# Optimization experiments

Measured on AMD Instinct MI355X. Metric: run time of the kernel, lower is better.

The kernel has to match this reference:

```python
import jax, jax.numpy as jnp
import numpy as np

D_MODEL = 1024
N_HEADS = 16
D_FF = 4096
D_K = D_MODEL // N_HEADS


def _ln(x, g, b, eps=1e-5):
    mu = jnp.mean(x, axis=-1, keepdims=True)
    var = jnp.mean(jnp.square(x - mu), axis=-1, keepdims=True)
    return (x - mu) * jax.lax.rsqrt(var + eps) * g + b


def setup_inputs() -> dict:
    key = jax.random.key(0)
    ks = jax.random.split(key, 16)
    s = 0.02
    inp = {
        "x": jax.random.normal(ks[0], (2, 2048, D_MODEL), dtype=jnp.float32),
        "Wq": jax.random.normal(ks[1], (D_MODEL, D_MODEL), dtype=jnp.float32) * s,
        "bq": jnp.zeros((D_MODEL,), jnp.float32),
        "Wk": jax.random.normal(ks[2], (D_MODEL, D_MODEL), dtype=jnp.float32) * s,
        "bk": jnp.zeros((D_MODEL,), jnp.float32),
        "Wv": jax.random.normal(ks[3], (D_MODEL, D_MODEL), dtype=jnp.float32) * s,
        "bv": jnp.zeros((D_MODEL,), jnp.float32),
        "Wo": jax.random.normal(ks[4], (D_MODEL, D_MODEL), dtype=jnp.float32) * s,
        "bo": jnp.zeros((D_MODEL,), jnp.float32),
        "W1": jax.random.normal(ks[5], (D_MODEL, D_FF), dtype=jnp.float32) * s,
        "b1": jnp.zeros((D_FF,), jnp.float32),
        "W2": jax.random.normal(ks[6], (D_FF, D_MODEL), dtype=jnp.float32) * s,
        "b2": jnp.zeros((D_MODEL,), jnp.float32),
        "g1": jnp.ones((D_MODEL,), jnp.float32),
        "be1": jnp.zeros((D_MODEL,), jnp.float32),
        "g2": jnp.ones((D_MODEL,), jnp.float32),
        "be2": jnp.zeros((D_MODEL,), jnp.float32),
    }
    return inp


def reference(x, Wq, bq, Wk, bk, Wv, bv, Wo, bo, W1, b1, W2, b2, g1, be1, g2, be2):
    B, L, D = x.shape
    # QKV projections -> [B, H, L, d_k]
    q = (x @ Wq + bq).reshape(B, L, N_HEADS, D_K).transpose(0, 2, 1, 3)
    k = (x @ Wk + bk).reshape(B, L, N_HEADS, D_K).transpose(0, 2, 1, 3)
    v = (x @ Wv + bv).reshape(B, L, N_HEADS, D_K).transpose(0, 2, 1, 3)
    scores = jnp.einsum("bhqd,bhkd->bhqk", q, k) / jnp.sqrt(jnp.float32(D_K))
    attn = jax.nn.softmax(scores, axis=-1)
    ctx = jnp.einsum("bhqk,bhkd->bhqd", attn, v)
    ctx = ctx.transpose(0, 2, 1, 3).reshape(B, L, D)
    attn_out = ctx @ Wo + bo
    # residual + LN1
    h = _ln(x + attn_out, g1, be1)
    # FFN (exact GELU, matching torch F.gelu default)
    ff = jax.nn.gelu(h @ W1 + b1, approximate=False) @ W2 + b2
    return _ln(h + ff, g2, be2)
```

## Files before the change

### kernel.cpp

```cpp
#include <hip/hip_runtime.h>
#include <cmath>


typedef unsigned short u16;
typedef unsigned int u32;
typedef __attribute__((ext_vector_type(8))) __bf16 bf16x8;
typedef __attribute__((ext_vector_type(4))) float f32x4;

#define MFMA16(a, b, c) __builtin_amdgcn_mfma_f32_16x16x32_bf16(a, b, c, 0, 0, 0)

__device__ __forceinline__ u16 f2bf(float f) {
  u32 u = __builtin_bit_cast(u32, f);
  u += 0x7fffu + ((u >> 16) & 1u);
  return (u16)(u >> 16);
}

__device__ __forceinline__ u32 packtrunc(float lo, float hi) {
#if __has_builtin(__builtin_amdgcn_perm)
  return __builtin_amdgcn_perm(__builtin_bit_cast(u32, hi),
                               __builtin_bit_cast(u32, lo), 0x07060302u);
#else
  return (__builtin_bit_cast(u32, lo) >> 16) |
         (__builtin_bit_cast(u32, hi) & 0xFFFF0000u);
#endif
}

__device__ __forceinline__ bf16x8 ld_frag(const u16* p) {
  return __builtin_bit_cast(bf16x8, *(const uint4*)p);
}

__device__ __forceinline__ float fexp2(float x) {
#if __has_builtin(__builtin_amdgcn_exp2f)
  return __builtin_amdgcn_exp2f(x);
#else
  return exp2f(x);
#endif
}

__device__ __forceinline__ float frcp(float x) {
#if __has_builtin(__builtin_amdgcn_rcpf)
  return __builtin_amdgcn_rcpf(x);
#else
  return 1.0f / x;
#endif
}

__device__ __forceinline__ float gelu_f(float v) {
  float x = v * 0.70710678118654752f;
  float a = fabsf(x);
  float t = frcp(fmaf(0.3275911f, a, 1.0f));
  float p = fmaf(1.061405429f, t, -1.453152027f);
  p = fmaf(p, t, 1.421413741f);
  p = fmaf(p, t, -0.284496736f);
  p = fmaf(p, t, 0.254829592f);
  p = p * t;
  float e = fexp2(-a * a * 1.4426950408889634f);
  float er = copysignf(1.0f - p * e, x);
  return 0.5f * v * (1.0f + er);
}

__device__ __forceinline__ void gload16(const u16* g, u16* l) {
  __builtin_amdgcn_global_load_lds(
      (const __attribute__((address_space(1))) void*)g,
      (__attribute__((address_space(3))) void*)l, 16, 0, 0);
}

#define WAITVL(N) asm volatile("s_waitcnt vmcnt(" #N ") lgkmcnt(0)" ::: "memory")
#define BAR() do { __builtin_amdgcn_s_barrier(); asm volatile("" ::: "memory"); } while (0)

__global__ __launch_bounds__(256) void prep_k(
    const float* __restrict__ x,
    const float* __restrict__ Wq, const float* __restrict__ Wk,
    const float* __restrict__ Wv, const float* __restrict__ Wo,
    const float* __restrict__ W1, const float* __restrict__ W2,
    u16* __restrict__ xb, u16* __restrict__ wqkvT, u16* __restrict__ woT,
    u16* __restrict__ w1T, u16* __restrict__ w2T) {
  const int z = blockIdx.z;
  if (z >= 12) {
    long i = (((long)(z - 12) * 1024 + blockIdx.y * 32 + blockIdx.x) * 256 +
              threadIdx.x) * 4;
    float4 v = *(const float4*)(x + i);
    ushort4 o;
    o.x = f2bf(v.x); o.y = f2bf(v.y); o.z = f2bf(v.z); o.w = f2bf(v.w);
    *(ushort4*)(xb + i) = o;
    return;
  }
  __shared__ float tile[32][33];
  const float* src;
  u16* dst;
  int R, C, r0, c0;
  if (z < 4) {
    src = (z == 0) ? Wq : (z == 1) ? Wk : (z == 2) ? Wv : Wo;
    dst = (z < 3) ? (wqkvT + (size_t)z * 1024 * 1024) : woT;
    R = 1024; C = 1024;
    r0 = blockIdx.y * 32; c0 = blockIdx.x * 32;
  } else if (z < 8) {
    src = W1; dst = w1T; R = 1024; C = 4096;
    r0 = blockIdx.y * 32; c0 = (z - 4) * 1024 + blockIdx.x * 32;
  } else {
    src = W2; dst = w2T; R = 4096; C = 1024;
    r0 = (z - 8) * 1024 + blockIdx.y * 32; c0 = blockIdx.x * 32;
  }
  int tx = threadIdx.x & 31, ty = threadIdx.x >> 5;
#pragma unroll
  for (int i = 0; i < 4; i++)
    tile[ty + 8 * i][tx] = src[(long)(r0 + ty + 8 * i) * C + c0 + tx];
  __syncthreads();
#pragma unroll
  for (int i = 0; i < 4; i++)
    dst[(long)(c0 + ty + 8 * i) * R + r0 + tx] = f2bf(tile[tx][ty + 8 * i]);
}

template <int MODE>
__global__ __launch_bounds__(512, 2) void gemm256_8p(
    const u16* __restrict__ A, const u16* __restrict__ BT,
    int N, int lda, int ldb, int K,
    const float* __restrict__ bias, u16* __restrict__ outB,
    u16* __restrict__ qd, u16* __restrict__ kd, u16* __restrict__ vTd,
    const float* __restrict__ bq, const float* __restrict__ bk,
    const float* __restrict__ bv) {
  __shared__ u16 As[2][2][128 * 64];
  __shared__ u16 Bs[2][2][128 * 64];
  const int tid = threadIdx.x;
  const int wave = tid >> 6, lane = tid & 63, quad = lane >> 4, l16 = lane & 15;
  const int wm = wave >> 2, wn = wave & 3;
  const int gx = gridDim.x;
  int flat = blockIdx.y * gx + blockIdx.x;
  const int cpx = (gx * gridDim.y) >> 3;
  flat = (flat & 7) * cpx + (flat >> 3);
  const int m0 = (flat / gx) * 256, n0 = (flat % gx) * 256;
  const int KT = K >> 6;

  const int srow8 = lane >> 3;
  const int sseg8 = (lane & 7) ^ srow8;
  const u16* aSrc = A + (long)(m0 + wave * 8 + srow8) * lda + sseg8 * 8;
  const u16* bSrc = BT + (long)(n0 + wave * 8 + srow8) * ldb + sseg8 * 8;

  auto stageA = [&](int tt, int h) {
    const u16* s = aSrc + (long)(h * 128) * lda + tt * 64;
    u16* d = &As[tt & 1][h][wave * 512];
    gload16(s, d);
    gload16(s + 64 * (long)lda, d + 4096);
  };
  auto stageB = [&](int tt, int h) {
    const u16* s = bSrc + (long)(h * 128) * ldb + tt * 64;
    u16* d = &Bs[tt & 1][h][wave * 512];
    gload16(s, d);
    gload16(s + 64 * (long)ldb, d + 4096);
  };

  const int s7 = l16 & 7;
  int lrB[4];
#pragma unroll
  for (int nf = 0; nf < 4; nf++) lrB[nf] = (wn & 1) * 64 + nf * 16 + l16;

  f32x4 acc[8][4] = {};

  stageA(0, 0); stageA(0, 1);
  stageB(0, 0); stageB(0, 1);
  stageA(1, 0); stageA(1, 1);
  stageB(1, 0); stageB(1, 1);
  WAITVL(8);
  BAR();

#pragma unroll 1
  for (int t = 0; t < KT; ++t) {
    const int buf = t & 1;
    const u16* Ah = &As[buf][wm][0];
    const u16* Bh = &Bs[buf][wn >> 1][0];
    bf16x8 bfr[4][2];
#pragma unroll
    for (int q = 0; q < 4; ++q) {
      if (q == 0) {
#pragma unroll
        for (int nf = 0; nf < 4; nf++)
#pragma unroll
          for (int kk = 0; kk < 2; kk++)
            bfr[nf][kk] =
                ld_frag(Bh + lrB[nf] * 64 + (((kk * 4 + quad) ^ s7) * 8));
      }
      bf16x8 af[2][2];
#pragma unroll
      for (int mfl = 0; mfl < 2; mfl++)
#pragma unroll
        for (int kk = 0; kk < 2; kk++)
          af[mfl][kk] = ld_frag(Ah + (q * 32 + mfl * 16 + l16) * 64 +
                                (((kk * 4 + quad) ^ s7) * 8));
      if (q == 0) { if (t >= 1 && t + 1 < KT) stageA(t + 1, 0); }
      else if (q == 1) { if (t >= 1 && t + 1 < KT) stageA(t + 1, 1); }
      else if (q == 2) { if (t + 2 < KT) stageB(t + 2, 0); }
      else {
        if (t + 2 < KT) stageB(t + 2, 1);
        if (t < KT - 2) { WAITVL(4); } else { WAITVL(0); }
      }
      BAR();
      __builtin_amdgcn_s_setprio(1);
#pragma unroll
      for (int kk = 0; kk < 2; kk++)
#pragma unroll
        for (int mfl = 0; mfl < 2; mfl++)
#pragma unroll
          for (int nf = 0; nf < 4; nf++)
            acc[q * 2 + mfl][nf] =
                MFMA16(af[mfl][kk], bfr[nf][kk], acc[q * 2 + mfl][nf]);
      __builtin_amdgcn_s_setprio(0);
      BAR();
    }
  }

  if (MODE == 0) {
    const int nbase = n0 + wn * 64;
    const int mat = nbase >> 10;
    const float* bp = (mat == 0) ? bq : ((mat == 1) ? bk : bv);
    float bb[4];
    int hh0[4], dd0[4];
#pragma unroll
    for (int nf = 0; nf < 4; nf++) {
      int nn = (nbase + nf * 16 + l16) & 1023;
      bb[nf] = bp[nn];
      hh0[nf] = nn >> 6;
      dd0[nf] = nn & 63;
    }
    if (mat < 2) {
#pragma unroll
      for (int mf = 0; mf < 8; mf++) {
#pragma unroll
        for (int r = 0; r < 4; r++) {
          int mr = m0 + wm * 128 + mf * 16 + quad * 4 + r;
          int bI = mr >> 11, ll = mr & 2047;
#pragma unroll
          for (int nf = 0; nf < 4; nf++) {
            float v = acc[mf][nf][r] + bb[nf];
            long idx = ((long)((bI * 16 + hh0[nf]) * 2048 + ll)) * 64 + dd0[nf];
            if (mat == 0) {
              qd[idx] = f2bf(v * 0.18033688011112043f);
            } else {
              kd[idx] = f2bf(v);
            }
          }
        }
      }
    } else {
#pragma unroll
      for (int nf = 0; nf < 4; nf++) {
#pragma unroll
        for (int mf = 0; mf < 8; mf++) {
#pragma unroll
          for (int r = 0; r < 4; r++) {
            int mr = m0 + wm * 128 + mf * 16 + quad * 4 + r;
            int bI = mr >> 11, ll = mr & 2047;
            float v = acc[mf][nf][r] + bb[nf];
            vTd[((long)((bI * 16 + hh0[nf]) * 64 + dd0[nf])) * 2048 + ll] = f2bf(v);
          }
        }
      }
    }
  } else {
    float bb[4];
#pragma unroll
    for (int nf = 0; nf < 4; nf++) bb[nf] = bias[n0 + wn * 64 + nf * 16 + l16];
#pragma unroll
    for (int mf = 0; mf < 8; mf++) {
#pragma unroll
      for (int r = 0; r < 4; r++) {
        int mr = m0 + wm * 128 + mf * 16 + quad * 4 + r;
        u16* orow = outB + (long)mr * N + n0 + wn * 64 + l16;
#pragma unroll
        for (int nf = 0; nf < 4; nf++)
          orow[nf * 16] = f2bf(gelu_f(acc[mf][nf][r] + bb[nf]));
      }
    }
  }
}

template <int MODE>
__global__ __launch_bounds__(256, 3) void gemm128_k(
    const u16* __restrict__ A, const u16* __restrict__ BT,
    int N, int lda, int ldb, int Kc,
    const float* __restrict__ bias, float* __restrict__ outF,
    u16* __restrict__ outB, float* __restrict__ p1) {
  __shared__ u16 As[3][128 * 32];
  __shared__ u16 Bs[3][128 * 32];
  const int tid = threadIdx.x;
  const int wave = tid >> 6, lane = tid & 63, quad = lane >> 4, l16 = lane & 15;
  const int wm = wave >> 1, wn = wave & 1;
  const int gx = gridDim.x;
  int flat = blockIdx.y * gx + blockIdx.x;
  const int cpx = (gx * gridDim.y) >> 3;
  flat = (flat & 7) * cpx + (flat >> 3);
  const int m0 = (flat / gx) * 128, n0 = (flat % gx) * 128;
  const int kz = blockIdx.z;
  const long kofs = (long)kz * Kc;
  const int KT = Kc >> 5;

  const int srow = lane >> 2;
  const int sseg = (lane & 3) ^ (srow & 3);
  const u16* aS = A + (long)(m0 + wave * 32 + srow) * lda + kofs + sseg * 8;
  const u16* bS = BT + (long)(n0 + wave * 32 + srow) * ldb + kofs + sseg * 8;

  auto stage = [&](int sb, int s) {
    const u16* pa = aS + (long)s * 32;
    gload16(pa, &As[sb][wave * 1024]);
    gload16(pa + 16 * (long)lda, &As[sb][wave * 1024 + 512]);
    const u16* pb = bS + (long)s * 32;
    gload16(pb, &Bs[sb][wave * 1024]);
    gload16(pb + 16 * (long)ldb, &Bs[sb][wave * 1024 + 512]);
  };

  int aro[4], bro[4];
#pragma unroll
  for (int f = 0; f < 4; f++) {
    int ra = wm * 64 + f * 16 + l16;
    aro[f] = ra * 32 + ((quad ^ (ra & 3)) * 8);
    int rb = wn * 64 + f * 16 + l16;
    bro[f] = rb * 32 + ((quad ^ (rb & 3)) * 8);
  }

  f32x4 acc[4][4] = {};

  stage(0, 0);
  stage(1, 1);
  int buf = 0;
#pragma unroll 1
  for (int t = 0; t < KT; ++t) {
    if (t < KT - 1) { WAITVL(4); } else { WAITVL(0); }
    BAR();
    bf16x8 af[4], bfr[4];
#pragma unroll
    for (int i = 0; i < 4; i++) af[i] = ld_frag(&As[buf][aro[i]]);
#pragma unroll
    for (int i = 0; i < 4; i++) bfr[i] = ld_frag(&Bs[buf][bro[i]]);
    if (t + 2 < KT) {
      int nb = buf + 2; if (nb >= 3) nb -= 3;
      stage(nb, t + 2);
    }
    __builtin_amdgcn_s_setprio(1);
#pragma unroll
    for (int mf = 0; mf < 4; mf++)
#pragma unroll
      for (int nf = 0; nf < 4; nf++)
        acc[mf][nf] = MFMA16(af[mf], bfr[nf], acc[mf][nf]);
    __builtin_amdgcn_s_setprio(0);
    if (++buf == 3) buf = 0;
  }

  {
    float* sl = (kz == 0) ? outF : p1;
#pragma unroll
    for (int mf = 0; mf < 4; mf++) {
#pragma unroll
      for (int r = 0; r < 4; r++) {
        int mr = m0 + wm * 64 + mf * 16 + quad * 4 + r;
        float* orow = sl + (long)mr * N + n0 + wn * 64 + l16;
#pragma unroll
        for (int nf = 0; nf < 4; nf++) orow[nf * 16] = acc[mf][nf][r];
      }
    }
  }
}

__global__ __launch_bounds__(256, 3) void attn_k(const u16* __restrict__ qd,
                                                 const u16* __restrict__ kd,
                                                 const u16* __restrict__ vTd,
                                                 u16* __restrict__ ctx) {
  __shared__ u16 Ks[2][64 * 64];
  __shared__ u16 Vs[2][64 * 64];
  __shared__ __align__(16) u16 P[4][32][72];
  const int tid = threadIdx.x;
  const int wave = tid >> 6, lane = tid & 63, quad = lane >> 4, l16 = lane & 15;
  const int bh = blockIdx.y;
  const u16* Q = qd + (long)bh * 2048 * 64;
  const u16* Kp = kd + (long)bh * 2048 * 64;
  const u16* Vt = vTd + (long)bh * 64 * 2048;
  const int qbase = blockIdx.x * 128 + wave * 32;

  bf16x8 qf[2][2];
#pragma unroll
  for (int qs = 0; qs < 2; qs++) {
    qf[qs][0] = ld_frag(Q + (qbase + qs * 16 + l16) * 64 + quad * 8);
    qf[qs][1] = ld_frag(Q + (qbase + qs * 16 + l16) * 64 + 32 + quad * 8);
  }

  f32x4 o[2][4] = {};
  float m[2] = {-1e30f, -1e30f}, l[2] = {0.f, 0.f};

  const int srow = lane >> 3;
  const int sx = (lane & 7) ^ srow;
  const int kr0 = wave * 16 + srow;
  const int kr1 = wave * 16 + 8 + srow;

  const int fs0 = ((0 * 4 + quad) ^ (l16 & 7)) * 8;
  const int fs1 = ((1 * 4 + quad) ^ (l16 & 7)) * 8;

  auto stage = [&](int buf, int j0) {
    gload16(Kp + (long)(j0 + kr0) * 64 + sx * 8, &Ks[buf][(wave * 2 + 0) * 512]);
    gload16(Kp + (long)(j0 + kr1) * 64 + sx * 8, &Ks[buf][(wave * 2 + 1) * 512]);
    gload16(Vt + (long)kr0 * 2048 + j0 + sx * 8, &Vs[buf][(wave * 2 + 0) * 512]);
    gload16(Vt + (long)kr1 * 2048 + j0 + sx * 8, &Vs[buf][(wave * 2 + 1) * 512]);
  };

  stage(0, 0);

#pragma unroll 1
  for (int j0 = 0; j0 < 2048; j0 += 64) {
    const int buf = (j0 >> 6) & 1;
    __syncthreads();
    if (j0 + 64 < 2048) stage(buf ^ 1, j0 + 64);

    const u16* kb = &Ks[buf][0];
    f32x4 st[2][4];
#pragma unroll
    for (int f = 0; f < 4; f++) {
      bf16x8 k0 = ld_frag(kb + (f * 16 + l16) * 64 + fs0);
      bf16x8 k1 = ld_frag(kb + (f * 16 + l16) * 64 + fs1);
      f32x4 s0 = {}, s1 = {};
      s0 = MFMA16(k0, qf[0][0], s0); s0 = MFMA16(k1, qf[0][1], s0);
      s1 = MFMA16(k0, qf[1][0], s1); s1 = MFMA16(k1, qf[1][1], s1);
      st[0][f] = s0; st[1][f] = s1;
    }

#pragma unroll
    for (int qs = 0; qs < 2; qs++) {
      float mx = -1e30f;
#pragma unroll
      for (int f = 0; f < 4; f++)
        mx = fmaxf(mx, fmaxf(fmaxf(st[qs][f][0], st[qs][f][1]),
                             fmaxf(st[qs][f][2], st[qs][f][3])));
      mx = fmaxf(mx, __shfl_xor(mx, 16));
      mx = fmaxf(mx, __shfl_xor(mx, 32));
      if (__any(mx > m[qs] + 8.0f)) {
        float mn = fmaxf(m[qs], mx);
        float al = fexp2(m[qs] - mn);
        m[qs] = mn;
        l[qs] *= al;
#pragma unroll
        for (int nt = 0; nt < 4; nt++) {
          o[qs][nt][0] *= al; o[qs][nt][1] *= al;
          o[qs][nt][2] *= al; o[qs][nt][3] *= al;
        }
      }
      float sm = 0.f;
      u16* prow = &P[wave][qs * 16 + l16][0];
#pragma unroll
      for (int f = 0; f < 4; f++) {
        float p0 = fexp2(st[qs][f][0] - m[qs]);
        float p1 = fexp2(st[qs][f][1] - m[qs]);
        float p2 = fexp2(st[qs][f][2] - m[qs]);
        float p3 = fexp2(st[qs][f][3] - m[qs]);
        sm += (p0 + p1) + (p2 + p3);
        uint2 u;
        u.x = packtrunc(p0, p1);
        u.y = packtrunc(p2, p3);
        *(uint2*)(prow + f * 16 + quad * 4) = u;
      }
      sm += __shfl_xor(sm, 16);
      sm += __shfl_xor(sm, 32);
      l[qs] += sm;
    }
    __asm__ volatile("s_waitcnt lgkmcnt(0)" ::: "memory");

    const u16* vb = &Vs[buf][0];
    bf16x8 vf[4][2];
#pragma unroll
    for (int nt = 0; nt < 4; nt++) {
      vf[nt][0] = ld_frag(vb + (nt * 16 + l16) * 64 + fs0);
      vf[nt][1] = ld_frag(vb + (nt * 16 + l16) * 64 + fs1);
    }
#pragma unroll
    for (int qs = 0; qs < 2; qs++) {
      const u16* prow = &P[wave][qs * 16 + l16][0];
#pragma unroll
      for (int kh = 0; kh < 2; kh++) {
        bf16x8 pf = ld_frag(prow + kh * 32 + quad * 8);
#pragma unroll
        for (int nt = 0; nt < 4; nt++)
          o[qs][nt] = MFMA16(vf[nt][kh], pf, o[qs][nt]);
      }
    }
  }

  const int bI = bh >> 4, hh = bh & 15;
#pragma unroll
  for (int qs = 0; qs < 2; qs++) {
    const float rl = 1.0f / l[qs];
    const long row = (long)(bI * 2048 + qbase + qs * 16 + l16);
#pragma unroll
    for (int nt = 0; nt < 4; nt++) {
      ushort4 w;
      w.x = f2bf(o[qs][nt][0] * rl);
      w.y = f2bf(o[qs][nt][1] * rl);
      w.z = f2bf(o[qs][nt][2] * rl);
      w.w = f2bf(o[qs][nt][3] * rl);
      *(ushort4*)(ctx + row * 1024 + hh * 64 + nt * 16 + quad * 4) = w;
    }
  }
}

__global__ __launch_bounds__(256) void ln2sb_k(const float* __restrict__ a,
                                               const float* __restrict__ q0,
                                               const float* __restrict__ q1,
                                               const float* __restrict__ bias,
                                               const float* __restrict__ g,
                                               const float* __restrict__ be,
                                               float* __restrict__ outF,
                                               u16* __restrict__ outB) {
  const int row = blockIdx.x, tid = threadIdx.x;
  const long base = (long)row * 1024;
  float v[4], s = 0.f, sq = 0.f;
#pragma unroll
  for (int i = 0; i < 4; i++) {
    int c = i * 256 + tid;
    float ff = q0[base + c] + q1[base + c] + bias[c];
    v[i] = a[base + c] + ff;
    s += v[i];
    sq += v[i] * v[i];
  }
#pragma unroll
  for (int off = 1; off < 64; off <<= 1) {
    s += __shfl_xor(s, off);
    sq += __shfl_xor(sq, off);
  }
  __shared__ float red[10];
  int wave = tid >> 6, lane = tid & 63;
  if (lane == 0) { red[wave * 2] = s; red[wave * 2 + 1] = sq; }
  __syncthreads();
  if (tid == 0) {
    float S = red[0] + red[2] + red[4] + red[6];
    float Q = red[1] + red[3] + red[5] + red[7];
    float mu = S * (1.0f / 1024.0f);
    float var = Q * (1.0f / 1024.0f) - mu * mu;
    red[8] = mu;
    red[9] = rsqrtf(var + 1e-5f);
  }
  __syncthreads();
  float mu = red[8], rstd = red[9];
#pragma unroll
  for (int i = 0; i < 4; i++) {
    int c = i * 256 + tid;
    float o = (v[i] - mu) * rstd * g[c] + be[c];
    outF[base + c] = o;
    if (outB) outB[base + c] = f2bf(o);
  }
}

extern "C" void kernel_launch(void* const* d_in, const int* in_sizes, int n_in,
                              void* d_out, int out_size, void* d_ws, size_t ws_size,
                              hipStream_t stream) {
  const float* x  = (const float*)d_in[0];
  const float* Wq = (const float*)d_in[1];  const float* bq = (const float*)d_in[2];
  const float* Wk = (const float*)d_in[3];  const float* bk = (const float*)d_in[4];
  const float* Wv = (const float*)d_in[5];  const float* bv = (const float*)d_in[6];
  const float* Wo = (const float*)d_in[7];  const float* bo = (const float*)d_in[8];
  const float* W1 = (const float*)d_in[9];  const float* b1 = (const float*)d_in[10];
  const float* W2 = (const float*)d_in[11]; const float* b2 = (const float*)d_in[12];
  const float* g1 = (const float*)d_in[13]; const float* be1 = (const float*)d_in[14];
  const float* g2 = (const float*)d_in[15]; const float* be2 = (const float*)d_in[16];

  char* ws = (char*)d_ws;
  size_t off = 0;
  auto alloc = [&](size_t bytes) {
    size_t o = off;
    off += (bytes + 255) & ~(size_t)255;
    return o;
  };
  u16*   xb     = (u16*)(ws + alloc(4096UL * 1024 * 2));
  u16*   wqkvT  = (u16*)(ws + alloc(3072UL * 1024 * 2));
  u16*   woT    = (u16*)(ws + alloc(1024UL * 1024 * 2));
  u16*   w1T    = (u16*)(ws + alloc(4096UL * 1024 * 2));
  u16*   w2T    = (u16*)(ws + alloc(1024UL * 4096 * 2));
  u16*   qb     = (u16*)(ws + alloc(32UL * 2048 * 64 * 2));
  u16*   kb     = (u16*)(ws + alloc(32UL * 2048 * 64 * 2));
  u16*   vTb    = (u16*)(ws + alloc(32UL * 64 * 2048 * 2));
  u16*   ctx    = (u16*)(ws + alloc(4096UL * 1024 * 2));
  float* attnO  = (float*)(ws + alloc(4096UL * 1024 * 4));
  float* h      = (float*)(ws + alloc(4096UL * 1024 * 4));
  u16*   hb     = (u16*)(ws + alloc(4096UL * 1024 * 2));
  u16*   ff1    = (u16*)(ws + alloc(4096UL * 4096 * 2));
  float* ff2    = (float*)(ws + alloc(4096UL * 1024 * 4));
  if (off > ws_size) return;

  float* wl0 = attnO;
  float* wl1 = ff2;
  float* sl0 = ff2;
  float* sl1 = attnO;

  prep_k<<<dim3(32, 32, 16), 256, 0, stream>>>(x, Wq, Wk, Wv, Wo, W1, W2,
                                               xb, wqkvT, woT, w1T, w2T);
  gemm256_8p<0><<<dim3(12, 16), 512, 0, stream>>>(
      xb, wqkvT, 3072, 1024, 1024, 1024,
      nullptr, nullptr, qb, kb, vTb, bq, bk, bv);
  attn_k<<<dim3(16, 32), 256, 0, stream>>>(qb, kb, vTb, ctx);
  gemm128_k<3><<<dim3(8, 32, 2), 256, 0, stream>>>(
      ctx, woT, 1024, 1024, 1024, 512,
      nullptr, wl0, nullptr, wl1);
  ln2sb_k<<<4096, 256, 0, stream>>>(x, wl0, wl1, bo, g1, be1, h, hb);
  gemm256_8p<2><<<dim3(16, 16), 512, 0, stream>>>(
      hb, w1T, 4096, 1024, 1024, 1024,
      b1, ff1, nullptr, nullptr, nullptr, nullptr, nullptr, nullptr);
  gemm128_k<3><<<dim3(8, 32, 2), 256, 0, stream>>>(
      ff1, w2T, 1024, 4096, 4096, 2048,
      nullptr, sl0, nullptr, sl1);
  ln2sb_k<<<4096, 256, 0, stream>>>(h, sl0, sl1, b2, g2, be2,
                                    (float*)d_out, nullptr);
}
```

Measured before the change: 356.5 us.

## Split-K W2 GEMM with 256-tile kernel and retile attention to 16-row waves

The FFN down-projection moves from the 128-tile split-K-by-2 kernel to the 256x256 eight-wave GEMM with a 4-way K split. Its fp32 partials are written into four buffers, reusing the dead q and vT buffers, and a new LayerNorm kernel sums all four. The attention kernel now runs 512 threads with 16 query rows per wave instead of 32, so each block has 8 waves for latency hiding. The trade-off is that K/V fragments are reused across fewer rows, and the split-K GEMM writes and reads more partial-sum traffic.

```diff
diff --git a/kernel.cpp b/kernel.cpp
--- a/kernel.cpp
+++ b/kernel.cpp
@@ -114,8 +114,10 @@
 template <int MODE>
 __global__ __launch_bounds__(512, 2) void gemm256_8p(
     const u16* __restrict__ A, const u16* __restrict__ BT,
-    int N, int lda, int ldb, int K,
+    int N, int lda, int ldb, int Kc,
     const float* __restrict__ bias, u16* __restrict__ outB,
+    float* __restrict__ outF, float* __restrict__ p1,
+    float* __restrict__ p2, float* __restrict__ p3,
     u16* __restrict__ qd, u16* __restrict__ kd, u16* __restrict__ vTd,
     const float* __restrict__ bq, const float* __restrict__ bk,
     const float* __restrict__ bv) {
@@ -129,12 +131,14 @@
   const int cpx = (gx * gridDim.y) >> 3;
   flat = (flat & 7) * cpx + (flat >> 3);
   const int m0 = (flat / gx) * 256, n0 = (flat % gx) * 256;
-  const int KT = K >> 6;
+  const int kz = blockIdx.z;
+  const long kofs = (long)kz * Kc;
+  const int KT = Kc >> 6;
 
   const int srow8 = lane >> 3;
   const int sseg8 = (lane & 7) ^ srow8;
-  const u16* aSrc = A + (long)(m0 + wave * 8 + srow8) * lda + sseg8 * 8;
-  const u16* bSrc = BT + (long)(n0 + wave * 8 + srow8) * ldb + sseg8 * 8;
+  const u16* aSrc = A + (long)(m0 + wave * 8 + srow8) * lda + kofs + sseg8 * 8;
+  const u16* bSrc = BT + (long)(n0 + wave * 8 + srow8) * ldb + kofs + sseg8 * 8;
 
   auto stageA = [&](int tt, int h) {
     const u16* s = aSrc + (long)(h * 128) * lda + tt * 64;
@@ -255,7 +259,7 @@
         }
       }
     }
-  } else {
+  } else if (MODE == 2) {
     float bb[4];
 #pragma unroll
     for (int nf = 0; nf < 4; nf++) bb[nf] = bias[n0 + wn * 64 + nf * 16 + l16];
@@ -268,6 +272,18 @@
 #pragma unroll
         for (int nf = 0; nf < 4; nf++)
           orow[nf * 16] = f2bf(gelu_f(acc[mf][nf][r] + bb[nf]));
+      }
+    }
+  } else {
+    float* sl = (kz == 0) ? outF : (kz == 1) ? p1 : (kz == 2) ? p2 : p3;
+#pragma unroll
+    for (int mf = 0; mf < 8; mf++) {
+#pragma unroll
+      for (int r = 0; r < 4; r++) {
+        int mr = m0 + wm * 128 + mf * 16 + quad * 4 + r;
+        float* orow = sl + (long)mr * N + n0 + wn * 64 + l16;
+#pragma unroll
+        for (int nf = 0; nf < 4; nf++) orow[nf * 16] = acc[mf][nf][r];
       }
     }
   }
@@ -359,44 +375,38 @@
   }
 }
 
-__global__ __launch_bounds__(256, 3) void attn_k(const u16* __restrict__ qd,
+__global__ __launch_bounds__(512, 4) void attn_k(const u16* __restrict__ qd,
                                                  const u16* __restrict__ kd,
                                                  const u16* __restrict__ vTd,
                                                  u16* __restrict__ ctx) {
   __shared__ u16 Ks[2][64 * 64];
   __shared__ u16 Vs[2][64 * 64];
-  __shared__ __align__(16) u16 P[4][32][72];
+  __shared__ __align__(16) u16 P[8][16][72];
   const int tid = threadIdx.x;
   const int wave = tid >> 6, lane = tid & 63, quad = lane >> 4, l16 = lane & 15;
   const int bh = blockIdx.y;
   const u16* Q = qd + (long)bh * 2048 * 64;
   const u16* Kp = kd + (long)bh * 2048 * 64;
   const u16* Vt = vTd + (long)bh * 64 * 2048;
-  const int qbase = blockIdx.x * 128 + wave * 32;
-
-  bf16x8 qf[2][2];
-#pragma unroll
-  for (int qs = 0; qs < 2; qs++) {
-    qf[qs][0] = ld_frag(Q + (qbase + qs * 16 + l16) * 64 + quad * 8);
-    qf[qs][1] = ld_frag(Q + (qbase + qs * 16 + l16) * 64 + 32 + quad * 8);
-  }
-
-  f32x4 o[2][4] = {};
-  float m[2] = {-1e30f, -1e30f}, l[2] = {0.f, 0.f};
+  const int qbase = blockIdx.x * 128 + wave * 16;
+
+  bf16x8 qf[2];
+  qf[0] = ld_frag(Q + (qbase + l16) * 64 + quad * 8);
+  qf[1] = ld_frag(Q + (qbase + l16) * 64 + 32 + quad * 8);
+
+  f32x4 o[4] = {};
+  float m = -1e30f, l = 0.f;
 
   const int srow = lane >> 3;
   const int sx = (lane & 7) ^ srow;
-  const int kr0 = wave * 16 + srow;
-  const int kr1 = wave * 16 + 8 + srow;
+  const int kr = wave * 8 + srow;
 
   const int fs0 = ((0 * 4 + quad) ^ (l16 & 7)) * 8;
   const int fs1 = ((1 * 4 + quad) ^ (l16 & 7)) * 8;
 
   auto stage = [&](int buf, int j0) {
-    gload16(Kp + (long)(j0 + kr0) * 64 + sx * 8, &Ks[buf][(wave * 2 + 0) * 512]);
-    gload16(Kp + (long)(j0 + kr1) * 64 + sx * 8, &Ks[buf][(wave * 2 + 1) * 512]);
-    gload16(Vt + (long)kr0 * 2048 + j0 + sx * 8, &Vs[buf][(wave * 2 + 0) * 512]);
-    gload16(Vt + (long)kr1 * 2048 + j0 + sx * 8, &Vs[buf][(wave * 2 + 1) * 512]);
+    gload16(Kp + (long)(j0 + kr) * 64 + sx * 8, &Ks[buf][wave * 512]);
+    gload16(Vt + (long)kr * 2048 + j0 + sx * 8, &Vs[buf][wave * 512]);
   };
 
   stage(0, 0);
@@ -408,91 +418,78 @@
     if (j0 + 64 < 2048) stage(buf ^ 1, j0 + 64);
 
     const u16* kb = &Ks[buf][0];
-    f32x4 st[2][4];
+    f32x4 st[4];
 #pragma unroll
     for (int f = 0; f < 4; f++) {
       bf16x8 k0 = ld_frag(kb + (f * 16 + l16) * 64 + fs0);
       bf16x8 k1 = ld_frag(kb + (f * 16 + l16) * 64 + fs1);
-      f32x4 s0 = {}, s1 = {};
-      s0 = MFMA16(k0, qf[0][0], s0); s0 = MFMA16(k1, qf[0][1], s0);
-      s1 = MFMA16(k0, qf[1][0], s1); s1 = MFMA16(k1, qf[1][1], s1);
-      st[0][f] = s0; st[1][f] = s1;
-    }
-
-#pragma unroll
-    for (int qs = 0; qs < 2; qs++) {
-      float mx = -1e30f;
-#pragma unroll
-      for (int f = 0; f < 4; f++)
-        mx = fmaxf(mx, fmaxf(fmaxf(st[qs][f][0], st[qs][f][1]),
-                             fmaxf(st[qs][f][2], st[qs][f][3])));
-      mx = fmaxf(mx, __shfl_xor(mx, 16));
-      mx = fmaxf(mx, __shfl_xor(mx, 32));
-      if (__any(mx > m[qs] + 8.0f)) {
-        float mn = fmaxf(m[qs], mx);
-        float al = fexp2(m[qs] - mn);
-        m[qs] = mn;
-        l[qs] *= al;
-#pragma unroll
-        for (int nt = 0; nt < 4; nt++) {
-          o[qs][nt][0] *= al; o[qs][nt][1] *= al;
-          o[qs][nt][2] *= al; o[qs][nt][3] *= al;
-        }
-      }
-      float sm = 0.f;
-      u16* prow = &P[wave][qs * 16 + l16][0];
-#pragma unroll
-      for (int f = 0; f < 4; f++) {
-        float p0 = fexp2(st[qs][f][0] - m[qs]);
-        float p1 = fexp2(st[qs][f][1] - m[qs]);
-        float p2 = fexp2(st[qs][f][2] - m[qs]);
-        float p3 = fexp2(st[qs][f][3] - m[qs]);
-        sm += (p0 + p1) + (p2 + p3);
-        uint2 u;
-        u.x = packtrunc(p0, p1);
-        u.y = packtrunc(p2, p3);
-        *(uint2*)(prow + f * 16 + quad * 4) = u;
-      }
-      sm += __shfl_xor(sm, 16);
-      sm += __shfl_xor(sm, 32);
-      l[qs] += sm;
-    }
+      f32x4 s0 = {};
+      s0 = MFMA16(k0, qf[0], s0);
+      s0 = MFMA16(k1, qf[1], s0);
+      st[f] = s0;
+    }
+
+    float mx = -1e30f;
+#pragma unroll
+    for (int f = 0; f < 4; f++)
+      mx = fmaxf(mx, fmaxf(fmaxf(st[f][0], st[f][1]),
+                           fmaxf(st[f][2], st[f][3])));
+    mx = fmaxf(mx, __shfl_xor(mx, 16));
+    mx = fmaxf(mx, __shfl_xor(mx, 32));
+    if (__any(mx > m + 8.0f)) {
+      float mn = fmaxf(m, mx);
+      float al = fexp2(m - mn);
+      m = mn;
+      l *= al;
+#pragma unroll
+      for (int nt = 0; nt < 4; nt++) {
+        o[nt][0] *= al; o[nt][1] *= al;
+        o[nt][2] *= al; o[nt][3] *= al;
+      }
+    }
+    float sm = 0.f;
+    u16* prow = &P[wave][l16][0];
+#pragma unroll
+    for (int f = 0; f < 4; f++) {
+      float p0 = fexp2(st[f][0] - m);
+      float p1 = fexp2(st[f][1] - m);
+      float p2 = fexp2(st[f][2] - m);
+      float p3 = fexp2(st[f][3] - m);
+      sm += (p0 + p1) + (p2 + p3);
+      uint2 u;
+      u.x = packtrunc(p0, p1);
+      u.y = packtrunc(p2, p3);
+      *(uint2*)(prow + f * 16 + quad * 4) = u;
+    }
+    sm += __shfl_xor(sm, 16);
+    sm += __shfl_xor(sm, 32);
+    l += sm;
     __asm__ volatile("s_waitcnt lgkmcnt(0)" ::: "memory");
 
     const u16* vb = &Vs[buf][0];
-    bf16x8 vf[4][2];
-#pragma unroll
-    for (int nt = 0; nt < 4; nt++) {
-      vf[nt][0] = ld_frag(vb + (nt * 16 + l16) * 64 + fs0);
-      vf[nt][1] = ld_frag(vb + (nt * 16 + l16) * 64 + fs1);
-    }
-#pragma unroll
-    for (int qs = 0; qs < 2; qs++) {
-      const u16* prow = &P[wave][qs * 16 + l16][0];
-#pragma unroll
-      for (int kh = 0; kh < 2; kh++) {
-        bf16x8 pf = ld_frag(prow + kh * 32 + quad * 8);
-#pragma unroll
-        for (int nt = 0; nt < 4; nt++)
-          o[qs][nt] = MFMA16(vf[nt][kh], pf, o[qs][nt]);
+#pragma unroll
+    for (int kh = 0; kh < 2; kh++) {
+      bf16x8 pf = ld_frag(prow + kh * 32 + quad * 8);
+      const int fsk = (kh == 0) ? fs0 : fs1;
+#pragma unroll
+      for (int nt = 0; nt < 4; nt++) {
+        bf16x8 vf = ld_frag(vb + (nt * 16 + l16) * 64 + fsk);
+        o[nt] = MFMA16(vf, pf, o[nt]);
       }
     }
   }
 
   const int bI = bh >> 4, hh = bh & 15;
-#pragma unroll
-  for (int qs = 0; qs < 2; qs++) {
-    const float rl = 1.0f / l[qs];
-    const long row = (long)(bI * 2048 + qbase + qs * 16 + l16);
-#pragma unroll
-    for (int nt = 0; nt < 4; nt++) {
-      ushort4 w;
-      w.x = f2bf(o[qs][nt][0] * rl);
-      w.y = f2bf(o[qs][nt][1] * rl);
-      w.z = f2bf(o[qs][nt][2] * rl);
-      w.w = f2bf(o[qs][nt][3] * rl);
-      *(ushort4*)(ctx + row * 1024 + hh * 64 + nt * 16 + quad * 4) = w;
-    }
+  const float rl = 1.0f / l;
+  const long row = (long)(bI * 2048 + qbase + l16);
+#pragma unroll
+  for (int nt = 0; nt < 4; nt++) {
+    ushort4 w;
+    w.x = f2bf(o[nt][0] * rl);
+    w.y = f2bf(o[nt][1] * rl);
+    w.z = f2bf(o[nt][2] * rl);
+    w.w = f2bf(o[nt][3] * rl);
+    *(ushort4*)(ctx + row * 1024 + hh * 64 + nt * 16 + quad * 4) = w;
   }
 }
 
@@ -540,6 +537,53 @@
     float o = (v[i] - mu) * rstd * g[c] + be[c];
     outF[base + c] = o;
     if (outB) outB[base + c] = f2bf(o);
+  }
+}
+
+__global__ __launch_bounds__(256) void ln4sb_k(const float* __restrict__ a,
+                                               const float* __restrict__ q0,
+                                               const float* __restrict__ q1,
+                                               const float* __restrict__ q2,
+                                               const float* __restrict__ q3,
+                                               const float* __restrict__ bias,
+                                               const float* __restrict__ g,
+                                               const float* __restrict__ be,
+                                               float* __restrict__ outF) {
+  const int row = blockIdx.x, tid = threadIdx.x;
+  const long base = (long)row * 1024;
+  float v[4], s = 0.f, sq = 0.f;
+#pragma unroll
+  for (int i = 0; i < 4; i++) {
+    int c = i * 256 + tid;
+    float ff = (q0[base + c] + q1[base + c]) + (q2[base + c] + q3[base + c]) +
+               bias[c];
+    v[i] = a[base + c] + ff;
+    s += v[i];
+    sq += v[i] * v[i];
+  }
+#pragma unroll
+  for (int off = 1; off < 64; off <<= 1) {
+    s += __shfl_xor(s, off);
+    sq += __shfl_xor(sq, off);
+  }
+  __shared__ float red[10];
+  int wave = tid >> 6, lane = tid & 63;
+  if (lane == 0) { red[wave * 2] = s; red[wave * 2 + 1] = sq; }
+  __syncthreads();
+  if (tid == 0) {
+    float S = red[0] + red[2] + red[4] + red[6];
+    float Q = red[1] + red[3] + red[5] + red[7];
+    float mu = S * (1.0f / 1024.0f);
+    float var = Q * (1.0f / 1024.0f) - mu * mu;
+    red[8] = mu;
+    red[9] = rsqrtf(var + 1e-5f);
+  }
+  __syncthreads();
+  float mu = red[8], rstd = red[9];
+#pragma unroll
+  for (int i = 0; i < 4; i++) {
+    int c = i * 256 + tid;
+    outF[base + c] = (v[i] - mu) * rstd * g[c] + be[c];
   }
 }
 
@@ -583,23 +627,28 @@
   float* wl1 = ff2;
   float* sl0 = ff2;
   float* sl1 = attnO;
+  float* sl2 = (float*)qb;
+  float* sl3 = (float*)vTb;
 
   prep_k<<<dim3(32, 32, 16), 256, 0, stream>>>(x, Wq, Wk, Wv, Wo, W1, W2,
                                                xb, wqkvT, woT, w1T, w2T);
   gemm256_8p<0><<<dim3(12, 16), 512, 0, stream>>>(
       xb, wqkvT, 3072, 1024, 1024, 1024,
-      nullptr, nullptr, qb, kb, vTb, bq, bk, bv);
-  attn_k<<<dim3(16, 32), 256, 0, stream>>>(qb, kb, vTb, ctx);
+      nullptr, nullptr, nullptr, nullptr, nullptr, nullptr,
+      qb, kb, vTb, bq, bk, bv);
+  attn_k<<<dim3(16, 32), 512, 0, stream>>>(qb, kb, vTb, ctx);
   gemm128_k<3><<<dim3(8, 32, 2), 256, 0, stream>>>(
       ctx, woT, 1024, 1024, 1024, 512,
       nullptr, wl0, nullptr, wl1);
   ln2sb_k<<<4096, 256, 0, stream>>>(x, wl0, wl1, bo, g1, be1, h, hb);
   gemm256_8p<2><<<dim3(16, 16), 512, 0, stream>>>(
       hb, w1T, 4096, 1024, 1024, 1024,
-      b1, ff1, nullptr, nullptr, nullptr, nullptr, nullptr, nullptr);
-  gemm128_k<3><<<dim3(8, 32, 2), 256, 0, stream>>>(
-      ff1, w2T, 1024, 4096, 4096, 2048,
-      nullptr, sl0, nullptr, sl1);
-  ln2sb_k<<<4096, 256, 0, stream>>>(h, sl0, sl1, b2, g2, be2,
-                                    (float*)d_out, nullptr);
-}
+      b1, ff1, nullptr, nullptr, nullptr, nullptr,
+      nullptr, nullptr, nullptr, nullptr, nullptr, nullptr);
+  gemm256_8p<3><<<dim3(4, 16, 4), 512, 0, stream>>>(
+      ff1, w2T, 1024, 4096, 4096, 1024,
+      nullptr, nullptr, sl0, sl1, sl2, sl3,
+      nullptr, nullptr, nullptr, nullptr, nullptr, nullptr);
+  ln4sb_k<<<4096, 256, 0, stream>>>(h, sl0, sl1, sl2, sl3, b2, g2, be2,
+                                    (float*)d_out);
+}
```

Measured after the change: 353.1 us. About the same (-1.0%).
